# Kernel optimization log

Measured on AMD Instinct MI355X. Metric: run time of the kernel, lower is better.

Reference implementation:

```python
import jax, jax.numpy as jnp
import numpy as np
from jax import lax

B, N, D, E, P, K, H = 32, 512, 512, 8, 96, 25, 4
PAD = 12  # conv padding so length is preserved


def setup_inputs() -> dict:
    key = jax.random.key(0)
    ks = jax.random.split(key, 16)
    s = 0.05  # weight scale to keep softmax/cosine well-conditioned
    x = jax.random.normal(ks[0], (B, N, D), dtype=jnp.float32)
    router = jax.random.normal(ks[1], (1, E, D), dtype=jnp.float32)
    Wq = jax.random.normal(ks[2], (D, D), dtype=jnp.float32) * s
    bq = jax.random.normal(ks[3], (D,), dtype=jnp.float32) * s
    Wk = jax.random.normal(ks[4], (D, D), dtype=jnp.float32) * s
    bk = jax.random.normal(ks[5], (D,), dtype=jnp.float32) * s
    Wv = jax.random.normal(ks[6], (D, D), dtype=jnp.float32) * s
    bv = jax.random.normal(ks[7], (D,), dtype=jnp.float32) * s
    Wo = jax.random.normal(ks[8], (D, D), dtype=jnp.float32) * s
    bo = jax.random.normal(ks[9], (D,), dtype=jnp.float32) * s
    Wc = jax.random.normal(ks[10], (E, 2, K), dtype=jnp.float32) * s  # E experts' Conv1d(2,1,25) stacked as out-channels
    bc = jax.random.normal(ks[11], (E,), dtype=jnp.float32) * s
    Wp = jax.random.normal(ks[12], (E, D, P), dtype=jnp.float32) * s  # E experts' Linear(D,P), stored (in,out)
    bp = jax.random.normal(ks[13], (E, P), dtype=jnp.float32) * s
    return {"x": x, "router": router, "Wq": Wq, "bq": bq, "Wk": Wk, "bk": bk,
            "Wv": Wv, "bv": bv, "Wo": Wo, "bo": bo, "Wc": Wc, "bc": bc,
            "Wp": Wp, "bp": bp}


def _forward(x, router, Wq, bq, Wk, bk, Wv, bv, Wo, bo, Wc, bc, Wp, bp):
    b, n, d = x.shape
    e = router.shape[1]
    dk = d // H
    r = jnp.broadcast_to(router, (b, e, d))
    # multi-head attention: queries=router slots, keys/values=x (dropout = identity at eval)
    q = (r @ Wq + bq).reshape(b, e, H, dk)
    k = (x @ Wk + bk).reshape(b, n, H, dk)
    v = (x @ Wv + bv).reshape(b, n, H, dk)
    scale = 1.0 / jnp.sqrt(jnp.asarray(dk, x.dtype))
    scores = jnp.einsum('blhe,bshe->bhls', q, k)  # [b,H,e,n]
    A = jax.nn.softmax(scale * scores, axis=-1)
    att = jnp.einsum('bhls,bshd->blhd', A, v).reshape(b, e, d)
    att = att @ Wo + bo  # [b,e,d]
    # cosine-similarity routing score, mapped to (1+pi)/2
    dot = jnp.einsum('bed,bnd->ben', att, x)
    norm_a = jnp.linalg.norm(att, axis=2, keepdims=True)          # [b,e,1]
    norm_x = jnp.linalg.norm(x, axis=2)[:, None, :]                # [b,1,n]
    score = (1.0 + dot / (norm_a * norm_x)) / 2.0                  # [b,e,n]
    idx = jnp.argmax(score, axis=1)                                # [b,n] expert per token
    z = jnp.take_along_axis(att, idx[:, :, None], axis=1)          # [b,n,d]
    result = jnp.stack([x, z], axis=-2).reshape(b * n, 2, d)       # [bn,2,d]
    # run all E expert convs at once (experts stacked as output channels)
    conv_out = lax.conv_general_dilated(
        result, Wc, window_strides=(1,), padding=[(PAD, PAD)],
        dimension_numbers=('NCH', 'OIH', 'NCH')) + bc[None, :, None]  # [bn,E,d]
    lin = jnp.einsum('nel,elp->nep', conv_out, Wp) + bp[None]         # [bn,E,P]
    flat_idx = idx.reshape(-1)
    out = jnp.take_along_axis(lin, flat_idx[:, None, None], axis=1)[:, 0, :]
    return out.reshape(b, n, P)


def reference(x, router, Wq, bq, Wk, bk, Wv, bv, Wo, bo, Wc, bc, Wp, bp):
    return _forward(x, router, Wq, bq, Wk, bk, Wv, bv, Wo, bo, Wc, bc, Wp, bp)
```

## Files before the change

### kernel.cpp

```cpp
#include <hip/hip_runtime.h>
#include <hip/hip_bf16.h>

#define B_ 32
#define N_ 512
#define D_ 512
#define E_ 8
#define P_ 96
#define KC 25
#define H_ 4
#define DK 128
#define HE 32
#define BN 16384

typedef short short8 __attribute__((ext_vector_type(8)));
typedef float f32x4 __attribute__((ext_vector_type(4)));

#define OCNT  4096
#define OS2   4352
#define OM    5120
#define OC    21504
#define OA    21536
#define OATT  676896
#define OTOK  807968
#define OWEFF 939040
#define OZC   1332256
#define OA1   5551136
#define OAP   16777216

__device__ __forceinline__ float b2f(short s) {
  unsigned u = ((unsigned)(unsigned short)s) << 16;
  return __builtin_bit_cast(float, u);
}
__device__ __forceinline__ unsigned short f2b(float f) {
  return __builtin_bit_cast(unsigned short, __float2bfloat16(f));
}

__global__ __launch_bounds__(256) void k_head(const float* __restrict__ router,
        const float* __restrict__ Wq, const float* __restrict__ bq,
        const float* __restrict__ Wk, const float* __restrict__ bk,
        const float* __restrict__ Wp,
        float* __restrict__ M, float* __restrict__ c,
        int* __restrict__ cnt, float* __restrict__ s2) {
  __shared__ float sm[896];
  int bid = blockIdx.x;
  int tid = threadIdx.x;
  if (bid < 64) {
    float* rs = sm;
    float* ps = sm + 512;
    float* qs = sm + 768;
    int he = bid >> 1, ch = bid & 1;
    int h = he >> 3, e = he & 7;
    for (int i = tid; i < 512; i += 256) rs[i] = router[e * D_ + i];
    __syncthreads();
    {
      int j = tid & 127, dh = tid >> 7;
      const float* wq = Wq + h * 128 + j;
      float acc = 0.f;
      for (int d = dh * 256; d < dh * 256 + 256; d += 4) {
        acc = fmaf(rs[d], wq[d * D_], acc);
        acc = fmaf(rs[d + 1], wq[(d + 1) * D_], acc);
        acc = fmaf(rs[d + 2], wq[(d + 2) * D_], acc);
        acc = fmaf(rs[d + 3], wq[(d + 3) * D_], acc);
      }
      ps[dh * 128 + j] = acc;
    }
    __syncthreads();
    if (tid < 128) qs[tid] = ps[tid] + ps[128 + tid] + bq[h * 128 + tid];
    __syncthreads();
    {
      int d0 = ch * 256 + tid;
      const float* wrow = Wk + d0 * D_ + h * 128;
      float acc = 0.f;
      for (int jj = 0; jj < 128; jj += 4) {
        float4 wv = *(const float4*)(wrow + jj);
        acc = fmaf(wv.x, qs[jj], acc);
        acc = fmaf(wv.y, qs[jj + 1], acc);
        acc = fmaf(wv.z, qs[jj + 2], acc);
        acc = fmaf(wv.w, qs[jj + 3], acc);
      }
      M[he * D_ + d0] = acc;
    }
    if (ch == 0 && tid < 64) {
      float s = qs[tid] * bk[h * 128 + tid] + qs[tid + 64] * bk[h * 128 + tid + 64];
#pragma unroll
      for (int off = 32; off; off >>= 1) s += __shfl_xor(s, off);
      if (tid == 0) c[he] = s;
    }
  } else {
    int e = bid - 64;
    if (bid == 64) cnt[tid] = 0;
    if (tid < 192) {
      int p = tid % 96, lg = tid / 96;
      float s = 0.f;
      const float* wp = Wp + e * D_ * P_ + p;
      for (int l = lg * 256; l < lg * 256 + 256; ++l) s += wp[l * P_];
      sm[lg * 96 + p] = s;
    }
    __syncthreads();
    if (tid < 96) s2[e * 96 + tid] = sm[tid] + sm[96 + tid];
  }
}

__global__ __launch_bounds__(128) void k_logits(const float* __restrict__ x,
        const float* __restrict__ M, float* __restrict__ A0,
        float* __restrict__ A1) {
  __shared__ float xs[64 * 132];
  __shared__ float Ms[32 * 132];
  int dh = blockIdx.x & 1;
  int nt8 = (blockIdx.x >> 1) & 7;
  int b = blockIdx.x >> 4;
  int tid = threadIdx.x;
  const float* xb = x + (b * N_ + nt8 * 64) * D_ + dh * 256;
  const float* Mb = M + dh * 256;
  float acc[4][4] = {{0.f}};
  for (int kc = 0; kc < 2; ++kc) {
    for (int idx = tid; idx < 2048; idx += 128) {
      int r = idx >> 5, c4 = (idx & 31) * 4;
      *(float4*)(xs + r * 132 + c4) = *(const float4*)(xb + r * D_ + kc * 128 + c4);
    }
    for (int idx = tid; idx < 1024; idx += 128) {
      int r = idx >> 5, c4 = (idx & 31) * 4;
      *(float4*)(Ms + r * 132 + c4) = *(const float4*)(Mb + r * D_ + kc * 128 + c4);
    }
    __syncthreads();
    int nt = tid & 15, ht = tid >> 4;
#pragma unroll 4
    for (int d4 = 0; d4 < 128; d4 += 4) {
      float4 xv[4], mv[4];
#pragma unroll
      for (int i = 0; i < 4; ++i)
        xv[i] = *(const float4*)(xs + (nt + 16 * i) * 132 + d4);
#pragma unroll
      for (int j = 0; j < 4; ++j)
        mv[j] = *(const float4*)(Ms + (ht + 8 * j) * 132 + d4);
#pragma unroll
      for (int i = 0; i < 4; ++i)
#pragma unroll
        for (int j = 0; j < 4; ++j) {
          float s = acc[i][j];
          s = fmaf(xv[i].x, mv[j].x, s);
          s = fmaf(xv[i].y, mv[j].y, s);
          s = fmaf(xv[i].z, mv[j].z, s);
          s = fmaf(xv[i].w, mv[j].w, s);
          acc[i][j] = s;
        }
    }
    __syncthreads();
  }
  int nt = tid & 15, ht = tid >> 4;
  float* Ad = dh ? A1 : A0;
#pragma unroll
  for (int j = 0; j < 4; ++j) {
    int he = ht + 8 * j;
#pragma unroll
    for (int i = 0; i < 4; ++i)
      Ad[(b * HE + he) * N_ + nt8 * 64 + nt + 16 * i] = acc[i][j];
  }
}

__global__ __launch_bounds__(512) void k_u(const float* __restrict__ x,
        const float* __restrict__ A0, const float* __restrict__ A1,
        const float* __restrict__ c, const float* __restrict__ Wv,
        const float* __restrict__ bv, const float* __restrict__ Wp,
        const float* __restrict__ Wc, __hip_bfloat16* __restrict__ weff,
        float* __restrict__ ap) {
  __shared__ __align__(16) char smem[49248];
  int tid = threadIdx.x;
  if (blockIdx.x >= 256) {
    float* T = (float*)smem;
    float* wcs = (float*)smem + 5760;
    int eb = blockIdx.x - 256;
    int e = eb >> 4, mc = eb & 15;
    int lo = mc * 32 - 12;
    for (int idx = tid; idx < 56 * 24; idx += 512) {
      int lp = idx / 24, p4 = (idx - lp * 24) * 4;
      int l = lo + lp;
      float4 v = {0.f, 0.f, 0.f, 0.f};
      if (l >= 0 && l < D_) v = *(const float4*)(Wp + (e * D_ + l) * P_ + p4);
      T[p4 * 60 + lp] = v.x; T[(p4 + 1) * 60 + lp] = v.y;
      T[(p4 + 2) * 60 + lp] = v.z; T[(p4 + 3) * 60 + lp] = v.w;
    }
    if (tid < 50) wcs[tid] = Wc[e * 2 * KC + tid];
    __syncthreads();
    if (tid < 256) {
      int m = tid & 31, pg = tid >> 5;
#pragma unroll
      for (int j = 0; j < 2; ++j)
        for (int k2 = 0; k2 < 12; ++k2) {
          int p = pg * 12 + k2;
          float acc = 0.f;
#pragma unroll
          for (int k = 0; k < KC; ++k)
            acc = fmaf(wcs[j * 25 + k], T[p * 60 + m - k + 24], acc);
          weff[(((e * 2 + j) * P_ + p) << 9) + mc * 32 + m] = __float2bfloat16(acc);
        }
    }
    return;
  }
  float* Ast  = (float*)smem;
  float* part = (float*)(smem + 8192);
  float* ust  = (float*)(smem + 40960);
  float* mH   = (float*)(smem + 49152);
  float* sH   = (float*)(smem + 49184);
  int id = blockIdx.x;
  int b = id & 31, g = id >> 5;
  int h = g >> 1, eb2 = (g & 1) * 4;
  const float scale = 0.08838834764831845f;
  int wv = tid >> 6, lane = tid & 63;
  int he_l = wv >> 1, half = wv & 1;
  float p[4];
  {
    int heg = g * 4 + he_l;
    const float* r0 = A0 + (b * HE + heg) * N_;
    const float* r1 = A1 + (b * HE + heg) * N_;
    float cc = c[heg];
    float v[4];
    float m = -1e30f;
#pragma unroll
    for (int k = 0; k < 4; ++k) {
      int n = half * 256 + lane + k * 64;
      float vv = scale * (r0[n] + r1[n] + cc);
      v[k] = vv;
      m = fmaxf(m, vv);
    }
    m = fmaxf(m, __shfl_xor(m, 1)); m = fmaxf(m, __shfl_xor(m, 2));
    m = fmaxf(m, __shfl_xor(m, 4)); m = fmaxf(m, __shfl_xor(m, 8));
    m = fmaxf(m, __shfl_xor(m, 16)); m = fmaxf(m, __shfl_xor(m, 32));
    if (lane == 0) mH[wv] = m;
    __syncthreads();
    m = fmaxf(mH[he_l * 2], mH[he_l * 2 + 1]);
    float s = 0.f;
#pragma unroll
    for (int k = 0; k < 4; ++k) { p[k] = expf(v[k] - m); s += p[k]; }
    s += __shfl_xor(s, 1); s += __shfl_xor(s, 2); s += __shfl_xor(s, 4);
    s += __shfl_xor(s, 8); s += __shfl_xor(s, 16); s += __shfl_xor(s, 32);
    if (lane == 0) sH[wv] = s;
  }
  __syncthreads();
  {
    float is_ = 1.0f / (sH[he_l * 2] + sH[he_l * 2 + 1]);
#pragma unroll
    for (int k = 0; k < 4; ++k) {
      int n = half * 256 + lane + k * 64;
      Ast[n * 4 + he_l] = p[k] * is_;
    }
  }
  __syncthreads();
  {
    int ns = tid >> 7, dg = tid & 127;
    float4 acc[4];
#pragma unroll
    for (int j = 0; j < 4; ++j) acc[j] = (float4){0.f, 0.f, 0.f, 0.f};
    const float* xb = x + (b * N_ + ns * 128) * D_ + dg * 4;
    const float* ab = Ast + ns * 128 * 4;
#pragma unroll 4
    for (int n = 0; n < 128; ++n) {
      float4 xv = *(const float4*)(xb + n * D_);
      float4 av = *(const float4*)(ab + n * 4);
      acc[0].x = fmaf(av.x, xv.x, acc[0].x); acc[0].y = fmaf(av.x, xv.y, acc[0].y);
      acc[0].z = fmaf(av.x, xv.z, acc[0].z); acc[0].w = fmaf(av.x, xv.w, acc[0].w);
      acc[1].x = fmaf(av.y, xv.x, acc[1].x); acc[1].y = fmaf(av.y, xv.y, acc[1].y);
      acc[1].z = fmaf(av.y, xv.z, acc[1].z); acc[1].w = fmaf(av.y, xv.w, acc[1].w);
      acc[2].x = fmaf(av.z, xv.x, acc[2].x); acc[2].y = fmaf(av.z, xv.y, acc[2].y);
      acc[2].z = fmaf(av.z, xv.z, acc[2].z); acc[2].w = fmaf(av.z, xv.w, acc[2].w);
      acc[3].x = fmaf(av.w, xv.x, acc[3].x); acc[3].y = fmaf(av.w, xv.y, acc[3].y);
      acc[3].z = fmaf(av.w, xv.z, acc[3].z); acc[3].w = fmaf(av.w, xv.w, acc[3].w);
    }
#pragma unroll
    for (int j = 0; j < 4; ++j)
      *(float4*)(part + ns * 2048 + j * 512 + dg * 4) = acc[j];
  }
  __syncthreads();
  {
    int d = tid;
    float4 s = {0.f, 0.f, 0.f, 0.f};
#pragma unroll
    for (int ns2 = 0; ns2 < 4; ++ns2) {
      s.x += part[ns2 * 2048 + 0 * 512 + d];
      s.y += part[ns2 * 2048 + 1 * 512 + d];
      s.z += part[ns2 * 2048 + 2 * 512 + d];
      s.w += part[ns2 * 2048 + 3 * 512 + d];
    }
    *(float4*)(ust + d * 4) = s;
  }
  __syncthreads();
  {
    int kq = tid >> 5, cg = tid & 31, c4 = cg * 4;
    float4 a2[4];
#pragma unroll
    for (int j = 0; j < 4; ++j) a2[j] = (float4){0.f, 0.f, 0.f, 0.f};
    const float* wvp = Wv + h * 128 + c4;
#pragma unroll 4
    for (int d = kq * 32; d < kq * 32 + 32; ++d) {
      float4 w4 = *(const float4*)(wvp + d * D_);
      float4 uu = *(const float4*)(ust + d * 4);
      a2[0].x = fmaf(uu.x, w4.x, a2[0].x); a2[0].y = fmaf(uu.x, w4.y, a2[0].y);
      a2[0].z = fmaf(uu.x, w4.z, a2[0].z); a2[0].w = fmaf(uu.x, w4.w, a2[0].w);
      a2[1].x = fmaf(uu.y, w4.x, a2[1].x); a2[1].y = fmaf(uu.y, w4.y, a2[1].y);
      a2[1].z = fmaf(uu.y, w4.z, a2[1].z); a2[1].w = fmaf(uu.y, w4.w, a2[1].w);
      a2[2].x = fmaf(uu.z, w4.x, a2[2].x); a2[2].y = fmaf(uu.z, w4.y, a2[2].y);
      a2[2].z = fmaf(uu.z, w4.z, a2[2].z); a2[2].w = fmaf(uu.z, w4.w, a2[2].w);
      a2[3].x = fmaf(uu.w, w4.x, a2[3].x); a2[3].y = fmaf(uu.w, w4.y, a2[3].y);
      a2[3].z = fmaf(uu.w, w4.z, a2[3].z); a2[3].w = fmaf(uu.w, w4.w, a2[3].w);
    }
#pragma unroll
    for (int j = 0; j < 4; ++j)
      *(float4*)(part + kq * 512 + j * 128 + c4) = a2[j];
  }
  __syncthreads();
  {
    int j = tid >> 7, cc = tid & 127;
    float s = 0.f;
#pragma unroll
    for (int kq2 = 0; kq2 < 16; ++kq2) s += part[kq2 * 512 + j * 128 + cc];
    ap[(b * E_ + eb2 + j) * D_ + h * 128 + cc] = s + bv[h * 128 + cc];
  }
}

__global__ __launch_bounds__(512) void k_op(const float* __restrict__ ap,
        const float* __restrict__ Wo, const float* __restrict__ bo,
        float* __restrict__ att) {
  __shared__ __align__(16) char smem[40960];
  float* apt  = (float*)smem;
  float* part = (float*)(smem + 8192);
  int id = blockIdx.x;
  int b = id & 31, q2 = id >> 5;
  int cq = q2 >> 1, eh = q2 & 1;
  int tid = threadIdx.x;
  {
    int j = tid >> 7, tl = tid & 127;
    const float* arow = ap + (b * E_ + eh * 4 + j) * D_;
#pragma unroll
    for (int k = 0; k < 4; ++k) {
      int i = tl + k * 128;
      apt[i * 4 + j] = arow[i];
    }
  }
  __syncthreads();
  {
    int kq = tid >> 5, cg = tid & 31, c4 = cg * 4;
    float4 a2[4];
#pragma unroll
    for (int j = 0; j < 4; ++j) a2[j] = (float4){0.f, 0.f, 0.f, 0.f};
    const float* wop = Wo + cq * 128 + c4;
#pragma unroll 4
    for (int d = kq * 32; d < kq * 32 + 32; ++d) {
      float4 w4 = *(const float4*)(wop + d * D_);
      float4 uu = *(const float4*)(apt + d * 4);
      a2[0].x = fmaf(uu.x, w4.x, a2[0].x); a2[0].y = fmaf(uu.x, w4.y, a2[0].y);
      a2[0].z = fmaf(uu.x, w4.z, a2[0].z); a2[0].w = fmaf(uu.x, w4.w, a2[0].w);
      a2[1].x = fmaf(uu.y, w4.x, a2[1].x); a2[1].y = fmaf(uu.y, w4.y, a2[1].y);
      a2[1].z = fmaf(uu.y, w4.z, a2[1].z); a2[1].w = fmaf(uu.y, w4.w, a2[1].w);
      a2[2].x = fmaf(uu.z, w4.x, a2[2].x); a2[2].y = fmaf(uu.z, w4.y, a2[2].y);
      a2[2].z = fmaf(uu.z, w4.z, a2[2].z); a2[2].w = fmaf(uu.z, w4.w, a2[2].w);
      a2[3].x = fmaf(uu.w, w4.x, a2[3].x); a2[3].y = fmaf(uu.w, w4.y, a2[3].y);
      a2[3].z = fmaf(uu.w, w4.z, a2[3].z); a2[3].w = fmaf(uu.w, w4.w, a2[3].w);
    }
#pragma unroll
    for (int j = 0; j < 4; ++j)
      *(float4*)(part + kq * 512 + j * 128 + c4) = a2[j];
  }
  __syncthreads();
  {
    int j = tid >> 7, cc = tid & 127;
    float s = 0.f;
#pragma unroll
    for (int kq2 = 0; kq2 < 16; ++kq2) s += part[kq2 * 512 + j * 128 + cc];
    att[(b * E_ + eh * 4 + j) * D_ + cq * 128 + cc] = s + bo[cq * 128 + cc];
  }
}

__global__ __launch_bounds__(512) void k_route2(const float* __restrict__ x,
        const float* __restrict__ att, const __hip_bfloat16* __restrict__ weff,
        const float* __restrict__ s2, const float* __restrict__ bc,
        const float* __restrict__ bp, int* __restrict__ cnt,
        int* __restrict__ tok, float* __restrict__ zc) {
  __shared__ float att_s[8 * D_];
  __shared__ float rn[8];
  __shared__ float red[8][520];
  __shared__ int blist[8][64];
  __shared__ int bcnt[8];
  int b = blockIdx.x >> 3, tile = blockIdx.x & 7;
  int tid = threadIdx.x;
  for (int idx = tid; idx < 1024; idx += 512)
    *(float4*)(att_s + idx * 4) = *(const float4*)(att + b * E_ * D_ + idx * 4);
  if (tid < 8) bcnt[tid] = 0;
  __syncthreads();
  if (tid < 256) {
    int e = tid >> 5, l = tid & 31;
    float s = 0.f;
    for (int d0 = l; d0 < D_; d0 += 32) {
      float v = att_s[e * D_ + d0];
      s = fmaf(v, v, s);
    }
#pragma unroll
    for (int off = 16; off; off >>= 1) s += __shfl_xor(s, off);
    if (l == 0) rn[e] = 1.0f / sqrtf(s);
  }
  __syncthreads();
  int w = tid >> 6, lane = tid & 63;
  int e2 = lane & 7, ch = lane >> 3;
  float* rw = red[w];
  for (int i = 0; i < 8; ++i) {
    int t = b * N_ + tile * 64 + w * 8 + i;
    const float* xp = x + t * D_ + lane * 8;
    float4 xa = *(const float4*)xp;
    float4 xb4 = *(const float4*)(xp + 4);
    float p[8];
#pragma unroll
    for (int e = 0; e < 8; ++e) {
      const float* apt = att_s + e * D_ + lane * 8;
      float4 a0 = *(const float4*)apt;
      float4 a1 = *(const float4*)(apt + 4);
      float s = a0.x * xa.x;
      s = fmaf(a0.y, xa.y, s); s = fmaf(a0.z, xa.z, s); s = fmaf(a0.w, xa.w, s);
      s = fmaf(a1.x, xb4.x, s); s = fmaf(a1.y, xb4.y, s);
      s = fmaf(a1.z, xb4.z, s); s = fmaf(a1.w, xb4.w, s);
      p[e] = s;
    }
#pragma unroll
    for (int e = 0; e < 8; ++e) rw[e * 65 + lane] = p[e];
    float s = 0.f;
#pragma unroll
    for (int k = 0; k < 8; ++k) s += rw[e2 * 65 + ch * 8 + k];
    s += __shfl_xor(s, 8); s += __shfl_xor(s, 16); s += __shfl_xor(s, 32);
    float sc = s * rn[e2];
    int be = e2;
#pragma unroll
    for (int off = 1; off < 8; off <<= 1) {
      float o = __shfl_xor(sc, off);
      int oe = __shfl_xor(be, off);
      if (o > sc || (o == sc && oe < be)) { sc = o; be = oe; }
    }
    if (lane == 0) {
      int slot = atomicAdd(&bcnt[be], 1);
      blist[be][slot] = t;
    }
  }
  __syncthreads();
  if (tid < 256) {
    int e = tid >> 5, r = tid & 31;
    int ce = bcnt[e];
    int gs = 0;
    if (r == 0 && ce > 0) gs = atomicAdd(&cnt[e * 32], ce);
    gs = __shfl(gs, (tid & 63) & 32);
    for (int k2 = r; k2 < ce; k2 += 32) tok[e * BN + gs + k2] = blist[e][k2];
  }
  int grp = tid >> 4, l16 = tid & 15;
  const float* arow = att_s + tile * D_;
  for (int r = 0; r < 3; ++r) {
    int p = r * 32 + grp;
    const short* wrow = (const short*)weff + (((tile * 2 + 1) * P_ + p) << 9);
    float acc = 0.f;
#pragma unroll
    for (int seg = 0; seg < 4; ++seg) {
      int d = seg * 128 + l16 * 8;
      short8 w8 = *(const short8*)(wrow + d);
      const float* a8 = arow + d;
      acc = fmaf(a8[0], b2f(w8[0]), acc); acc = fmaf(a8[1], b2f(w8[1]), acc);
      acc = fmaf(a8[2], b2f(w8[2]), acc); acc = fmaf(a8[3], b2f(w8[3]), acc);
      acc = fmaf(a8[4], b2f(w8[4]), acc); acc = fmaf(a8[5], b2f(w8[5]), acc);
      acc = fmaf(a8[6], b2f(w8[6]), acc); acc = fmaf(a8[7], b2f(w8[7]), acc);
    }
    acc += __shfl_xor(acc, 1); acc += __shfl_xor(acc, 2);
    acc += __shfl_xor(acc, 4); acc += __shfl_xor(acc, 8);
    if (l16 == 0)
      zc[(b * E_ + tile) * P_ + p] = acc + bc[tile] * s2[tile * 96 + p]
                                     + bp[tile * 96 + p];
  }
}

__global__ __launch_bounds__(256) void k_final(const float* __restrict__ x,
        const __hip_bfloat16* __restrict__ weff, const float* __restrict__ zc,
        const int* __restrict__ cnt, const int* __restrict__ tok,
        float* __restrict__ out) {
  __shared__ __align__(16) unsigned short xsb[32 * 520];
  __shared__ int toks[32];
  int g = blockIdx.x;
  int cl_e[E_], bs[E_ + 1];
  bs[0] = 0;
#pragma unroll
  for (int e = 0; e < E_; ++e) {
    cl_e[e] = cnt[e * 32];
    bs[e + 1] = bs[e] + ((cl_e[e] + 31) >> 5);
  }
  if (g >= bs[E_]) return;
  int e = 0;
#pragma unroll
  for (int k = 1; k < E_; ++k) if (g >= bs[k]) e = k;
  int base = (g - bs[e]) * 32;
  int cnt_e = cl_e[e];
  int cl = cnt_e - base; if (cl > 32) cl = 32;
  int tid = threadIdx.x;
  if (tid < 32) toks[tid] = (tid < cl) ? tok[e * BN + base + tid] : tok[e * BN + base];
  __syncthreads();
  for (int idx = tid; idx < 32 * 128; idx += 256) {
    int r = idx >> 7, c4 = (idx & 127) * 4;
    float4 v = *(const float4*)(x + toks[r] * D_ + c4);
    ushort4 u4;
    u4.x = f2b(v.x); u4.y = f2b(v.y); u4.z = f2b(v.z); u4.w = f2b(v.w);
    *(ushort4*)(xsb + r * 520 + c4) = u4;
  }
  __syncthreads();
  int wave = tid >> 6, lane = tid & 63;
  int mw = wave & 1, nw = wave >> 1;
  int m16 = lane & 15, quad = lane >> 4;
  const short* w0 = (const short*)(weff + (e * 2 + 0) * P_ * D_);
  f32x4 acc[3];
#pragma unroll
  for (int nt = 0; nt < 3; ++nt) acc[nt] = (f32x4){0.f, 0.f, 0.f, 0.f};
  const short* arow = (const short*)xsb + (mw * 16 + m16) * 520 + quad * 8;
  const short* brow = w0 + (nw * 48 + m16) * D_ + quad * 8;
  for (int kt = 0; kt < 16; ++kt) {
    int koff = kt * 32;
    short8 a = *(const short8*)(arow + koff);
#pragma unroll
    for (int nt = 0; nt < 3; ++nt) {
      short8 bf = *(const short8*)(brow + nt * 16 * D_ + koff);
      acc[nt] = __builtin_amdgcn_mfma_f32_16x16x32_bf16(a, bf, acc[nt], 0, 0, 0);
    }
  }
#pragma unroll
  for (int nt = 0; nt < 3; ++nt)
#pragma unroll
    for (int rr = 0; rr < 4; ++rr) {
      int row = mw * 16 + quad * 4 + rr;
      if (row < cl) {
        int tg = toks[row];
        int bb = tg >> 9;
        int p = nw * 48 + nt * 16 + m16;
        out[tg * P_ + p] = acc[nt][rr] + zc[(bb * E_ + e) * P_ + p];
      }
    }
}

extern "C" void kernel_launch(void* const* d_in, const int* in_sizes, int n_in,
                              void* d_out, int out_size, void* d_ws, size_t ws_size,
                              hipStream_t stream) {
  const float* x      = (const float*)d_in[0];
  const float* router = (const float*)d_in[1];
  const float* Wq     = (const float*)d_in[2];
  const float* bq     = (const float*)d_in[3];
  const float* Wk     = (const float*)d_in[4];
  const float* bk     = (const float*)d_in[5];
  const float* Wv     = (const float*)d_in[6];
  const float* bv     = (const float*)d_in[7];
  const float* Wo     = (const float*)d_in[8];
  const float* bo     = (const float*)d_in[9];
  const float* Wc     = (const float*)d_in[10];
  const float* bc     = (const float*)d_in[11];
  const float* Wp     = (const float*)d_in[12];
  const float* bp     = (const float*)d_in[13];
  float* out = (float*)d_out;
  float* w = (float*)d_ws;

  int*   cnt  = (int*)(w + OCNT);
  float* s2   = w + OS2;
  float* M    = w + OM;
  float* c    = w + OC;
  float* A0   = w + OA;
  float* A1   = w + OA1;
  float* att  = w + OATT;
  int*   tok  = (int*)(w + OTOK);
  __hip_bfloat16* weff = (__hip_bfloat16*)(w + OWEFF);
  float* zc   = w + OZC;
  float* ap   = w + OAP;

  k_head<<<72, 256, 0, stream>>>(router, Wq, bq, Wk, bk, Wp, M, c, cnt, s2);
  k_logits<<<512, 128, 0, stream>>>(x, M, A0, A1);
  k_u<<<384, 512, 0, stream>>>(x, A0, A1, c, Wv, bv, Wp, Wc, weff, ap);
  k_op<<<256, 512, 0, stream>>>(ap, Wo, bo, att);
  k_route2<<<256, 512, 0, stream>>>(x, att, weff, s2, bc, bp, cnt, tok, zc);
  k_final<<<520, 256, 0, stream>>>(x, weff, zc, cnt, tok, out);
}
```

Baseline: 199.1 us.

## Fuse output projection into k_u via atomics and move weff build to k_logits

Removes the separate k_op kernel by having each k_u block multiply its per-head partial attention output by its 128-row slice of Wo and atomically accumulate into att. att is zeroed in extra k_head blocks, and the bo bias is added later when k_route2 loads att. The effective conv-linear weight (weff) construction moves from k_u into extra k_logits blocks, so it runs alongside the logits work. This saves a kernel launch and the ap round trip, but adds float atomics, which are contended and make summation order nondeterministic.

Result: no change. 200.0 us (+0.5%).

```diff
diff --git a/kernel.cpp b/kernel.cpp
--- a/kernel.cpp
+++ b/kernel.cpp
@@ -25,7 +25,6 @@
 #define OWEFF 939040
 #define OZC   1332256
 #define OA1   5551136
-#define OAP   16777216
 
 __device__ __forceinline__ float b2f(short s) {
   unsigned u = ((unsigned)(unsigned short)s) << 16;
@@ -40,7 +39,8 @@
         const float* __restrict__ Wk, const float* __restrict__ bk,
         const float* __restrict__ Wp,
         float* __restrict__ M, float* __restrict__ c,
-        int* __restrict__ cnt, float* __restrict__ s2) {
+        int* __restrict__ cnt, float* __restrict__ s2,
+        float* __restrict__ att) {
   __shared__ float sm[896];
   int bid = blockIdx.x;
   int tid = threadIdx.x;
@@ -86,7 +86,7 @@
       for (int off = 32; off; off >>= 1) s += __shfl_xor(s, off);
       if (tid == 0) c[he] = s;
     }
-  } else {
+  } else if (bid < 72) {
     int e = bid - 64;
     if (bid == 64) cnt[tid] = 0;
     if (tid < 192) {
@@ -98,18 +98,54 @@
     }
     __syncthreads();
     if (tid < 96) s2[e * 96 + tid] = sm[tid] + sm[96 + tid];
+  } else {
+    float* ab = att + (bid - 72) * 16384 + tid * 4;
+    float4 z = {0.f, 0.f, 0.f, 0.f};
+#pragma unroll
+    for (int k = 0; k < 16; ++k) *(float4*)(ab + k * 1024) = z;
   }
 }
 
 __global__ __launch_bounds__(128) void k_logits(const float* __restrict__ x,
         const float* __restrict__ M, float* __restrict__ A0,
-        float* __restrict__ A1) {
+        float* __restrict__ A1, const float* __restrict__ Wp,
+        const float* __restrict__ Wc, __hip_bfloat16* __restrict__ weff) {
   __shared__ float xs[64 * 132];
   __shared__ float Ms[32 * 132];
+  int tid = threadIdx.x;
+  if (blockIdx.x >= 512) {
+    float* T = xs;
+    float* wcs = xs + 5800;
+    int eb = blockIdx.x - 512;
+    int e = eb >> 4, mc = eb & 15;
+    int lo = mc * 32 - 12;
+    for (int idx = tid; idx < 56 * 24; idx += 128) {
+      int lp = idx / 24, p4 = (idx - lp * 24) * 4;
+      int l = lo + lp;
+      float4 v = {0.f, 0.f, 0.f, 0.f};
+      if (l >= 0 && l < D_) v = *(const float4*)(Wp + (e * D_ + l) * P_ + p4);
+      T[p4 * 60 + lp] = v.x; T[(p4 + 1) * 60 + lp] = v.y;
+      T[(p4 + 2) * 60 + lp] = v.z; T[(p4 + 3) * 60 + lp] = v.w;
+    }
+    if (tid < 50) wcs[tid] = Wc[e * 2 * KC + tid];
+    __syncthreads();
+    int m = tid & 31, pg4 = tid >> 5;
+    for (int pp = pg4; pp < 8; pp += 4)
+#pragma unroll
+      for (int j = 0; j < 2; ++j)
+        for (int k2 = 0; k2 < 12; ++k2) {
+          int p = pp * 12 + k2;
+          float acc = 0.f;
+#pragma unroll
+          for (int k = 0; k < KC; ++k)
+            acc = fmaf(wcs[j * 25 + k], T[p * 60 + m - k + 24], acc);
+          weff[(((e * 2 + j) * P_ + p) << 9) + mc * 32 + m] = __float2bfloat16(acc);
+        }
+    return;
+  }
   int dh = blockIdx.x & 1;
   int nt8 = (blockIdx.x >> 1) & 7;
   int b = blockIdx.x >> 4;
-  int tid = threadIdx.x;
   const float* xb = x + (b * N_ + nt8 * 64) * D_ + dh * 256;
   const float* Mb = M + dh * 256;
   float acc[4][4] = {{0.f}};
@@ -161,47 +197,15 @@
 __global__ __launch_bounds__(512) void k_u(const float* __restrict__ x,
         const float* __restrict__ A0, const float* __restrict__ A1,
         const float* __restrict__ c, const float* __restrict__ Wv,
-        const float* __restrict__ bv, const float* __restrict__ Wp,
-        const float* __restrict__ Wc, __hip_bfloat16* __restrict__ weff,
-        float* __restrict__ ap) {
+        const float* __restrict__ bv, const float* __restrict__ Wo,
+        float* __restrict__ att) {
   __shared__ __align__(16) char smem[49248];
-  int tid = threadIdx.x;
-  if (blockIdx.x >= 256) {
-    float* T = (float*)smem;
-    float* wcs = (float*)smem + 5760;
-    int eb = blockIdx.x - 256;
-    int e = eb >> 4, mc = eb & 15;
-    int lo = mc * 32 - 12;
-    for (int idx = tid; idx < 56 * 24; idx += 512) {
-      int lp = idx / 24, p4 = (idx - lp * 24) * 4;
-      int l = lo + lp;
-      float4 v = {0.f, 0.f, 0.f, 0.f};
-      if (l >= 0 && l < D_) v = *(const float4*)(Wp + (e * D_ + l) * P_ + p4);
-      T[p4 * 60 + lp] = v.x; T[(p4 + 1) * 60 + lp] = v.y;
-      T[(p4 + 2) * 60 + lp] = v.z; T[(p4 + 3) * 60 + lp] = v.w;
-    }
-    if (tid < 50) wcs[tid] = Wc[e * 2 * KC + tid];
-    __syncthreads();
-    if (tid < 256) {
-      int m = tid & 31, pg = tid >> 5;
-#pragma unroll
-      for (int j = 0; j < 2; ++j)
-        for (int k2 = 0; k2 < 12; ++k2) {
-          int p = pg * 12 + k2;
-          float acc = 0.f;
-#pragma unroll
-          for (int k = 0; k < KC; ++k)
-            acc = fmaf(wcs[j * 25 + k], T[p * 60 + m - k + 24], acc);
-          weff[(((e * 2 + j) * P_ + p) << 9) + mc * 32 + m] = __float2bfloat16(acc);
-        }
-    }
-    return;
-  }
   float* Ast  = (float*)smem;
   float* part = (float*)(smem + 8192);
   float* ust  = (float*)(smem + 40960);
   float* mH   = (float*)(smem + 49152);
   float* sH   = (float*)(smem + 49184);
+  int tid = threadIdx.x;
   int id = blockIdx.x;
   int b = id & 31, g = id >> 5;
   int h = g >> 1, eb2 = (g & 1) * 4;
@@ -308,70 +312,49 @@
       *(float4*)(part + kq * 512 + j * 128 + c4) = a2[j];
   }
   __syncthreads();
+  float* apbT = ust;
   {
     int j = tid >> 7, cc = tid & 127;
     float s = 0.f;
 #pragma unroll
     for (int kq2 = 0; kq2 < 16; ++kq2) s += part[kq2 * 512 + j * 128 + cc];
-    ap[(b * E_ + eb2 + j) * D_ + h * 128 + cc] = s + bv[h * 128 + cc];
-  }
-}
-
-__global__ __launch_bounds__(512) void k_op(const float* __restrict__ ap,
-        const float* __restrict__ Wo, const float* __restrict__ bo,
-        float* __restrict__ att) {
-  __shared__ __align__(16) char smem[40960];
-  float* apt  = (float*)smem;
-  float* part = (float*)(smem + 8192);
-  int id = blockIdx.x;
-  int b = id & 31, q2 = id >> 5;
-  int cq = q2 >> 1, eh = q2 & 1;
-  int tid = threadIdx.x;
-  {
-    int j = tid >> 7, tl = tid & 127;
-    const float* arow = ap + (b * E_ + eh * 4 + j) * D_;
-#pragma unroll
-    for (int k = 0; k < 4; ++k) {
-      int i = tl + k * 128;
-      apt[i * 4 + j] = arow[i];
-    }
-  }
-  __syncthreads();
-  {
-    int kq = tid >> 5, cg = tid & 31, c4 = cg * 4;
-    float4 a2[4];
-#pragma unroll
-    for (int j = 0; j < 4; ++j) a2[j] = (float4){0.f, 0.f, 0.f, 0.f};
-    const float* wop = Wo + cq * 128 + c4;
+    apbT[cc * 4 + j] = s + bv[h * 128 + cc];
+  }
+  __syncthreads();
+  {
+    int cc = tid;
+    const float* wo = Wo + (h * 128) * D_ + cc;
+    float e0 = 0.f, e1 = 0.f, e2 = 0.f, e3 = 0.f;
 #pragma unroll 4
-    for (int d = kq * 32; d < kq * 32 + 32; ++d) {
-      float4 w4 = *(const float4*)(wop + d * D_);
-      float4 uu = *(const float4*)(apt + d * 4);
-      a2[0].x = fmaf(uu.x, w4.x, a2[0].x); a2[0].y = fmaf(uu.x, w4.y, a2[0].y);
-      a2[0].z = fmaf(uu.x, w4.z, a2[0].z); a2[0].w = fmaf(uu.x, w4.w, a2[0].w);
-      a2[1].x = fmaf(uu.y, w4.x, a2[1].x); a2[1].y = fmaf(uu.y, w4.y, a2[1].y);
-      a2[1].z = fmaf(uu.y, w4.z, a2[1].z); a2[1].w = fmaf(uu.y, w4.w, a2[1].w);
-      a2[2].x = fmaf(uu.z, w4.x, a2[2].x); a2[2].y = fmaf(uu.z, w4.y, a2[2].y);
-      a2[2].z = fmaf(uu.z, w4.z, a2[2].z); a2[2].w = fmaf(uu.z, w4.w, a2[2].w);
-      a2[3].x = fmaf(uu.w, w4.x, a2[3].x); a2[3].y = fmaf(uu.w, w4.y, a2[3].y);
-      a2[3].z = fmaf(uu.w, w4.z, a2[3].z); a2[3].w = fmaf(uu.w, w4.w, a2[3].w);
-    }
-#pragma unroll
-    for (int j = 0; j < 4; ++j)
-      *(float4*)(part + kq * 512 + j * 128 + c4) = a2[j];
-  }
-  __syncthreads();
-  {
-    int j = tid >> 7, cc = tid & 127;
-    float s = 0.f;
-#pragma unroll
-    for (int kq2 = 0; kq2 < 16; ++kq2) s += part[kq2 * 512 + j * 128 + cc];
-    att[(b * E_ + eh * 4 + j) * D_ + cq * 128 + cc] = s + bo[cq * 128 + cc];
+    for (int d4 = 0; d4 < 128; d4 += 4) {
+      float w0 = wo[(d4 + 0) * D_];
+      float w1 = wo[(d4 + 1) * D_];
+      float w2 = wo[(d4 + 2) * D_];
+      float w3 = wo[(d4 + 3) * D_];
+      float4 a0 = *(const float4*)(apbT + (d4 + 0) * 4);
+      float4 a1 = *(const float4*)(apbT + (d4 + 1) * 4);
+      float4 a2 = *(const float4*)(apbT + (d4 + 2) * 4);
+      float4 a3 = *(const float4*)(apbT + (d4 + 3) * 4);
+      e0 = fmaf(a0.x, w0, e0); e0 = fmaf(a1.x, w1, e0);
+      e0 = fmaf(a2.x, w2, e0); e0 = fmaf(a3.x, w3, e0);
+      e1 = fmaf(a0.y, w0, e1); e1 = fmaf(a1.y, w1, e1);
+      e1 = fmaf(a2.y, w2, e1); e1 = fmaf(a3.y, w3, e1);
+      e2 = fmaf(a0.z, w0, e2); e2 = fmaf(a1.z, w1, e2);
+      e2 = fmaf(a2.z, w2, e2); e2 = fmaf(a3.z, w3, e2);
+      e3 = fmaf(a0.w, w0, e3); e3 = fmaf(a1.w, w1, e3);
+      e3 = fmaf(a2.w, w2, e3); e3 = fmaf(a3.w, w3, e3);
+    }
+    float* ab = att + (b * E_ + eb2) * D_ + cc;
+    atomicAdd(ab, e0);
+    atomicAdd(ab + D_, e1);
+    atomicAdd(ab + 2 * D_, e2);
+    atomicAdd(ab + 3 * D_, e3);
   }
 }
 
 __global__ __launch_bounds__(512) void k_route2(const float* __restrict__ x,
-        const float* __restrict__ att, const __hip_bfloat16* __restrict__ weff,
+        const float* __restrict__ att, const float* __restrict__ bo,
+        const __hip_bfloat16* __restrict__ weff,
         const float* __restrict__ s2, const float* __restrict__ bc,
         const float* __restrict__ bp, int* __restrict__ cnt,
         int* __restrict__ tok, float* __restrict__ zc) {
@@ -382,8 +365,12 @@
   __shared__ int bcnt[8];
   int b = blockIdx.x >> 3, tile = blockIdx.x & 7;
   int tid = threadIdx.x;
-  for (int idx = tid; idx < 1024; idx += 512)
-    *(float4*)(att_s + idx * 4) = *(const float4*)(att + b * E_ * D_ + idx * 4);
+  for (int idx = tid; idx < 1024; idx += 512) {
+    float4 av = *(const float4*)(att + b * E_ * D_ + idx * 4);
+    float4 bv4 = *(const float4*)(bo + ((idx * 4) & 511));
+    av.x += bv4.x; av.y += bv4.y; av.z += bv4.z; av.w += bv4.w;
+    *(float4*)(att_s + idx * 4) = av;
+  }
   if (tid < 8) bcnt[tid] = 0;
   __syncthreads();
   if (tid < 256) {
@@ -564,12 +551,10 @@
   int*   tok  = (int*)(w + OTOK);
   __hip_bfloat16* weff = (__hip_bfloat16*)(w + OWEFF);
   float* zc   = w + OZC;
-  float* ap   = w + OAP;
-
-  k_head<<<72, 256, 0, stream>>>(router, Wq, bq, Wk, bk, Wp, M, c, cnt, s2);
-  k_logits<<<512, 128, 0, stream>>>(x, M, A0, A1);
-  k_u<<<384, 512, 0, stream>>>(x, A0, A1, c, Wv, bv, Wp, Wc, weff, ap);
-  k_op<<<256, 512, 0, stream>>>(ap, Wo, bo, att);
-  k_route2<<<256, 512, 0, stream>>>(x, att, weff, s2, bc, bp, cnt, tok, zc);
+
+  k_head<<<80, 256, 0, stream>>>(router, Wq, bq, Wk, bk, Wp, M, c, cnt, s2, att);
+  k_logits<<<640, 128, 0, stream>>>(x, M, A0, A1, Wp, Wc, weff);
+  k_u<<<256, 512, 0, stream>>>(x, A0, A1, c, Wv, bv, Wo, att);
+  k_route2<<<256, 512, 0, stream>>>(x, att, bo, weff, s2, bc, bp, cnt, tok, zc);
   k_final<<<520, 256, 0, stream>>>(x, weff, zc, cnt, tok, out);
 }
```
